# Kernel tuning notes

Measured on AMD Instinct MI355X. Metric: run time of the kernel, lower is better.

The kernel has to match this reference:

```python
import jax, jax.numpy as jnp
import numpy as np

N = 50000


def cheb_conv(x, row, col, deg_inv_sqrt, diag_w, W, b):
    """PyG ChebConv with K=3, normalization='sym', lambda_max=2.
    L~ = 2L/lambda_max - I = -D^{-1/2} A D^{-1/2} (diag 0 for deg>0, -1 for isolated).
    T0 = x, T1 = L~ x, T2 = 2 L~ T1 - T0; out = sum_k Tk @ W[k] + b.
    """
    w = -deg_inv_sqrt[row] * deg_inv_sqrt[col]  # [E]

    def Lhat(h):
        # message: w_e * h[src], aggregated at dst (source_to_target flow)
        agg = jax.ops.segment_sum(w[:, None] * h[col], row, num_segments=N)
        return agg + diag_w[:, None] * h

    Tx0 = x
    Tx1 = Lhat(x)
    Tx2 = 2.0 * Lhat(Tx1) - Tx0
    return Tx0 @ W[0] + Tx1 @ W[1] + Tx2 @ W[2] + b


def setup_inputs() -> dict:
    key = jax.random.key(0)
    ks = jax.random.split(key, 8)
    x = jax.random.normal(ks[0], (N, 512), dtype=jnp.float32)
    edge_index = jax.random.randint(ks[1], (2, 1600000), 0, N, dtype=jnp.int64)
    w1 = jax.random.normal(ks[2], (3, 512, 250), dtype=jnp.float32) * 0.05
    b1 = jnp.zeros((250,), dtype=jnp.float32)
    w2 = jax.random.normal(ks[3], (3, 250, 500), dtype=jnp.float32) * 0.05
    b2 = jnp.zeros((500,), dtype=jnp.float32)
    w3 = jax.random.normal(ks[4], (3, 500, 1000), dtype=jnp.float32) * 0.05
    b3 = jnp.zeros((1000,), dtype=jnp.float32)
    return {"x": x, "edge_index": edge_index, "w1": w1, "b1": b1,
            "w2": w2, "b2": b2, "w3": w3, "b3": b3}


def reference(x, edge_index, w1, b1, w2, b2, w3, b3):
    row, col = edge_index[1], edge_index[0]  # dst, src (source_to_target)
    # symmetric-normalization degree (computed as in PyG get_laplacian: scatter on row)
    deg = jax.ops.segment_sum(jnp.ones(edge_index.shape[1], dtype=x.dtype), row,
                              num_segments=N)
    deg_inv_sqrt = jnp.where(deg > 0, jax.lax.rsqrt(jnp.maximum(deg, 1.0)), 0.0)
    diag_w = jnp.where(deg > 0, 0.0, -1.0).astype(x.dtype)  # 2*L_ii/lmax - 1

    h = jax.nn.relu(cheb_conv(x, row, col, deg_inv_sqrt, diag_w, w1, b1))
    h = jax.nn.relu(cheb_conv(h, row, col, deg_inv_sqrt, diag_w, w2, b2))
    h = jax.nn.relu(cheb_conv(h, row, col, deg_inv_sqrt, diag_w, w3, b3))
    return h
```

## Files before the change

### kernel.cpp

```cpp
#include <hip/hip_runtime.h>


typedef unsigned short u16;
typedef __attribute__((ext_vector_type(8))) short s16x8;
typedef __attribute__((ext_vector_type(4))) float f32x4;
typedef __attribute__((ext_vector_type(8))) unsigned short u16x8;
typedef __attribute__((ext_vector_type(4))) unsigned short u16x4;
typedef __attribute__((ext_vector_type(8))) signed char s8x8;
typedef __attribute__((ext_vector_type(4))) signed char s8x4;

__device__ __forceinline__ float b2f(u16 u) {
  union { unsigned int i; float f; } x; x.i = ((unsigned int)u) << 16; return x.f;
}
__device__ __forceinline__ u16 f2b(float f) {
  union { float f; unsigned int i; } x; x.f = f;
  unsigned int r = x.i + 0x7fffu + ((x.i >> 16) & 1u);
  return (u16)(r >> 16);
}

typedef __attribute__((address_space(1))) unsigned int gu32_t;
typedef __attribute__((address_space(3))) unsigned int lu32_t;
__device__ __forceinline__ void gload16(const void* g, void* l) {
  __builtin_amdgcn_global_load_lds((const gu32_t*)g, (lu32_t*)l, 16, 0, 0);
}

__global__ void k_zero_i32(int* p, int n) {
  int t = blockIdx.x * 256 + threadIdx.x;
  if (t < n) p[t] = 0;
}

__global__ void k_hist(const int* __restrict__ ei, int* __restrict__ cnt, int E) {
  int e = blockIdx.x * 256 + threadIdx.x;
  if (e < E) atomicAdd(&cnt[ei[E + e]], 1);
}

__global__ void k_dis(const int* __restrict__ cnt, float* __restrict__ dis, int N) {
  int t = blockIdx.x * 256 + threadIdx.x;
  if (t < N) dis[t] = cnt[t] > 0 ? rsqrtf((float)cnt[t]) : 0.f;
}

__global__ void k_scan1(const int* __restrict__ cnt, int* __restrict__ part, int N) {
  __shared__ int s[256];
  int t = threadIdx.x, idx = blockIdx.x * 256 + t;
  s[t] = idx < N ? cnt[idx] : 0;
  __syncthreads();
  for (int o = 128; o > 0; o >>= 1) {
    if (t < o) s[t] += s[t + o];
    __syncthreads();
  }
  if (t == 0) part[blockIdx.x] = s[0];
}

__global__ void k_scan2(int* part, int nb, int* csroff, int N, int E) {
  if (threadIdx.x == 0 && blockIdx.x == 0) {
    int run = 0;
    for (int b = 0; b < nb; ++b) { int v = part[b]; part[b] = run; run += v; }
    csroff[N] = E;
  }
}

__global__ void k_scan3(const int* __restrict__ cnt, const int* __restrict__ part,
                        int* __restrict__ csroff, int* __restrict__ cursor, int N) {
  __shared__ int s[256];
  int t = threadIdx.x, idx = blockIdx.x * 256 + t;
  int v = idx < N ? cnt[idx] : 0;
  s[t] = v;
  __syncthreads();
  for (int o = 1; o < 256; o <<= 1) {
    int add = t >= o ? s[t - o] : 0;
    __syncthreads();
    s[t] += add;
    __syncthreads();
  }
  if (idx < N) {
    int ex = part[blockIdx.x] + s[t] - v;
    csroff[idx] = ex;
    cursor[idx] = ex;
  }
}

__global__ void k_scatter(const int* __restrict__ ei, int* __restrict__ cursor,
                          int* __restrict__ csrsrc, int E) {
  int e = blockIdx.x * 256 + threadIdx.x;
  if (e >= E) return;
  int s = ei[e];
  int d = ei[E + e];
  int pos = atomicAdd(&cursor[d], 1);
  csrsrc[pos] = s;
}

__global__ void k_convx(const float* __restrict__ x, u16* __restrict__ C, int N, int NPAD) {
  int t = blockIdx.x * 256 + threadIdx.x;
  int row = t >> 6;
  if (row >= NPAD) return;
  int c0 = (t & 63) * 8;
  u16x8 o;
  if (row < N) {
    const float4* p = (const float4*)(x + (size_t)row * 512 + c0);
    float4 a = p[0], b = p[1];
    o[0] = f2b(a.x); o[1] = f2b(a.y); o[2] = f2b(a.z); o[3] = f2b(a.w);
    o[4] = f2b(b.x); o[5] = f2b(b.y); o[6] = f2b(b.z); o[7] = f2b(b.w);
  } else {
#pragma unroll
    for (int j = 0; j < 8; ++j) o[j] = 0;
  }
  *(u16x8*)(C + (size_t)row * 512 + c0) = o;
}

__global__ void k_convw_kblk(const float* __restrict__ W, u16* __restrict__ Wb,
                             int Fin, int Kpad, int Nout) {
  int n = blockIdx.x;
  int ldw = 3 * Kpad;
  for (int kk = threadIdx.x; kk < ldw; kk += 256) {
    int ck = kk / Kpad, k = kk - ck * Kpad;
    float v = (k < Fin && n < Nout) ? W[((size_t)ck * Fin + k) * Nout + n] : 0.f;
    Wb[(size_t)n * ldw + kk] = f2b(v);
  }
}

__global__ void k_convw_nblk(const float* __restrict__ W, u16* __restrict__ Wb,
                             int Nout ) {
  int n = blockIdx.x;
  int ck = n >> 8, j = n & 255;
  for (int k = threadIdx.x; k < 512; k += 256) {
    float v = (j < Nout) ? W[((size_t)ck * 512 + k) * Nout + j] : 0.f;
    Wb[(size_t)n * 512 + k] = f2b(v);
  }
}

template <int FV>
__global__ __launch_bounds__(256) void k_quant(
    const u16* __restrict__ T, int ldt, signed char* __restrict__ Q, int ldq,
    const float* __restrict__ dis, float* __restrict__ qs, float* __restrict__ sc,
    int N) {
  using uvec = typename
      __hip_internal::conditional<FV == 8, u16x8, u16x4>::type;
  using qvec = typename
      __hip_internal::conditional<FV == 8, s8x8, s8x4>::type;
  const int r = blockIdx.x * 4 + (threadIdx.x >> 6);
  if (r >= N) return;
  const int l = threadIdx.x & 63, c0 = l * FV;
  const uvec v = *(const uvec*)(T + (size_t)r * ldt + c0);
  float f[FV];
  float m = 0.f;
#pragma unroll
  for (int j = 0; j < FV; ++j) { f[j] = b2f(v[j]); m = fmaxf(m, fabsf(f[j])); }
#pragma unroll
  for (int o = 32; o > 0; o >>= 1) m = fmaxf(m, __shfl_xor(m, o, 64));
  const float inv = m > 0.f ? 127.f / m : 0.f;
  qvec q;
#pragma unroll
  for (int j = 0; j < FV; ++j) q[j] = (signed char)(int)rintf(f[j] * inv);
  *(qvec*)(Q + (size_t)r * ldq + c0) = q;
  if (l == 0) {
    const float s = m > 0.f ? m * (1.f / 127.f) : 0.f;
    sc[r] = s;
    qs[r] = dis[r] * s;
  }
}

template <int FV, int MODE>
__global__ __launch_bounds__(256) void spmm_q(
    const signed char* __restrict__ Q, int ldq,
    const float* __restrict__ qs, const float* __restrict__ sc,
    const u16* __restrict__ E0, const u16* __restrict__ E1, int lde,
    const float* __restrict__ bias, int nreal,
    u16* __restrict__ O, int ldo,
    const int* __restrict__ off, const int* __restrict__ srcs,
    const float* __restrict__ dis, int N) {
  using uvec = typename
      __hip_internal::conditional<FV == 8, u16x8, u16x4>::type;
  using qvec = typename
      __hip_internal::conditional<FV == 8, s8x8, s8x4>::type;
  const int r = blockIdx.x * 4 + (threadIdx.x >> 6);
  if (r >= N) return;
  const int c0 = (threadIdx.x & 63) * FV;
  const signed char* __restrict__ Qc = Q + c0;
  float acc[FV];
#pragma unroll
  for (int j = 0; j < FV; ++j) acc[j] = 0.f;
  int e = off[r];
  const int e1 = off[r + 1];
  for (; e + 4 <= e1; e += 4) {
    const int s0 = srcs[e], s1 = srcs[e + 1], s2 = srcs[e + 2], s3 = srcs[e + 3];
    const float w0 = qs[s0], w1 = qs[s1], w2 = qs[s2], w3 = qs[s3];
    const qvec v0 = *(const qvec*)(Qc + (size_t)s0 * ldq);
    const qvec v1 = *(const qvec*)(Qc + (size_t)s1 * ldq);
    const qvec v2 = *(const qvec*)(Qc + (size_t)s2 * ldq);
    const qvec v3 = *(const qvec*)(Qc + (size_t)s3 * ldq);
#pragma unroll
    for (int j = 0; j < FV; ++j)
      acc[j] += w0 * (float)v0[j] + w1 * (float)v1[j] +
                w2 * (float)v2[j] + w3 * (float)v3[j];
  }
  for (; e < e1; ++e) {
    const int s0 = srcs[e];
    const float w0 = qs[s0];
    const qvec v0 = *(const qvec*)(Qc + (size_t)s0 * ldq);
#pragma unroll
    for (int j = 0; j < FV; ++j) acc[j] += w0 * (float)v0[j];
  }
  const float disr = dis[r];
  float lap[FV];
#pragma unroll
  for (int j = 0; j < FV; ++j) lap[j] = -disr * acc[j];
  if (disr == 0.f) {
    const float s = sc[r];
    const qvec v = *(const qvec*)(Qc + (size_t)r * ldq);
#pragma unroll
    for (int j = 0; j < FV; ++j) lap[j] -= s * (float)v[j];
  }
  uvec o;
  if constexpr (MODE == 0) {
#pragma unroll
    for (int j = 0; j < FV; ++j) o[j] = f2b(lap[j]);
  } else if constexpr (MODE == 1) {
    const uvec h = *(const uvec*)(E0 + (size_t)r * lde + c0);
#pragma unroll
    for (int j = 0; j < FV; ++j) o[j] = f2b(2.f * lap[j] - b2f(h[j]));
  } else if constexpr (MODE == 2) {
    const uvec u1 = *(const uvec*)(E0 + (size_t)r * lde + c0);
#pragma unroll
    for (int j = 0; j < FV; ++j) o[j] = f2b(b2f(u1[j]) + 2.f * lap[j]);
  } else {
    const uvec u0 = *(const uvec*)(E0 + (size_t)r * lde + c0);
    const uvec u2 = *(const uvec*)(E1 + (size_t)r * lde + c0);
#pragma unroll
    for (int j = 0; j < FV; ++j) {
      const int c = c0 + j;
      const float bv = (c < nreal) ? bias[c] : 0.f;
      float v = b2f(u0[j]) - b2f(u2[j]) + lap[j] + bv;
      o[j] = f2b(v > 0.f ? v : 0.f);
    }
  }
  *(uvec*)(O + (size_t)r * ldo + c0) = o;
}

template <typename OUTT, bool ACT>
__global__ __launch_bounds__(256) void gemm_k(
    const u16* __restrict__ A, int lda,
    const u16* __restrict__ B, int ldb,
    const float* __restrict__ bias,
    OUTT* __restrict__ C, int ldc,
    int K, int nmask, int nreal, int Nrows, int NT) {
  __shared__ u16 As[128 * 64];
  __shared__ u16 Bs[128 * 64];
  const int tid = threadIdx.x;
  const int w = tid >> 6, l = tid & 63;

  const int nwg = gridDim.x;
  const int q = nwg >> 3, r8 = nwg & 7;
  const int xcd = blockIdx.x & 7, idx = blockIdx.x >> 3;
  const int wg = (xcd < r8 ? xcd * (q + 1) : r8 * (q + 1) + (xcd - r8) * q) + idx;
  const int m0 = (wg / NT) * 128, n0 = (wg % NT) * 128;

  const int srow = w * 8 + (l >> 3);
  const int scol = ((l & 7) ^ (l >> 3)) * 8;
  const u16* ga = A + (size_t)m0 * lda + scol;
  const u16* gb = B + (size_t)n0 * ldb + scol;
  u16* lAs = &As[w * 512];
  u16* lBs = &Bs[w * 512];

  f32x4 acc[4][4];
#pragma unroll
  for (int m = 0; m < 4; ++m)
#pragma unroll
    for (int n = 0; n < 4; ++n) acc[m][n] = (f32x4){0.f, 0.f, 0.f, 0.f};

  const int wr = (w >> 1) * 64, wc = (w & 1) * 64;
  const int tr = l & 15, tg = l >> 4;
  const int rx = tr & 7;

  for (int k0 = 0; k0 < K; k0 += 64) {
    __syncthreads();
#pragma unroll
    for (int c = 0; c < 4; ++c) {
      gload16(ga + (size_t)(srow + c * 32) * lda + k0, lAs + c * 2048);
      gload16(gb + (size_t)(srow + c * 32) * ldb + k0, lBs + c * 2048);
    }
    __syncthreads();
#pragma unroll
    for (int kk = 0; kk < 64; kk += 32) {
      s16x8 af[4], bf[4];
#pragma unroll
      for (int m = 0; m < 4; ++m)
        af[m] = *(const s16x8*)&As[(wr + m * 16 + tr) * 64 + ((((kk >> 3) + tg) ^ rx) * 8)];
#pragma unroll
      for (int n = 0; n < 4; ++n)
        bf[n] = *(const s16x8*)&Bs[(wc + n * 16 + tr) * 64 + ((((kk >> 3) + tg) ^ rx) * 8)];
#pragma unroll
      for (int m = 0; m < 4; ++m)
#pragma unroll
        for (int n = 0; n < 4; ++n)
          acc[m][n] = __builtin_amdgcn_mfma_f32_16x16x32_bf16(af[m], bf[n], acc[m][n], 0, 0, 0);
    }
  }

#pragma unroll
  for (int m = 0; m < 4; ++m) {
    const int gr0 = m0 + wr + m * 16 + tg * 4;
#pragma unroll
    for (int n = 0; n < 4; ++n) {
      const int gc = n0 + wc + n * 16 + tr;
      const bool cv = (gc & nmask) < nreal;
      const float bv = (ACT && cv) ? bias[gc] : 0.f;
#pragma unroll
      for (int j = 0; j < 4; ++j) {
        float v = acc[m][n][j] + bv;
        if (ACT) v = v > 0.f ? v : 0.f;
        if constexpr (sizeof(OUTT) == 2) {
          C[(size_t)(gr0 + j) * ldc + gc] = cv ? f2b(v) : (u16)0;
        } else {
          if (gr0 + j < Nrows && cv)
            C[(size_t)(gr0 + j) * ldc + gc] = v;
        }
      }
    }
  }
}

extern "C" void kernel_launch(void* const* d_in, const int* in_sizes, int n_in,
                              void* d_out, int out_size, void* d_ws, size_t ws_size,
                              hipStream_t stream) {
  const float* x = (const float*)d_in[0];
  const int* ei = (const int*)d_in[1];
  const float* w1 = (const float*)d_in[2];
  const float* b1 = (const float*)d_in[3];
  const float* w2 = (const float*)d_in[4];
  const float* b2 = (const float*)d_in[5];
  const float* w3 = (const float*)d_in[6];
  const float* b3 = (const float*)d_in[7];
  float* out = (float*)d_out;

  const int N = in_sizes[0] / 512;
  const int E = in_sizes[1] / 2;
  const int NPAD = ((N + 127) / 128) * 128;
  const int NB = (N + 255) / 256;
  const int EB = (E + 255) / 256;
  const int MT = NPAD / 128;

  char* ws = (char*)d_ws;
  size_t o = 0;
  auto alloc = [&](size_t b) -> void* {
    void* p = ws + o;
    o = (o + b + 255) & ~(size_t)255;
    return p;
  };
  int* cnt = (int*)alloc((size_t)N * 4);
  float* dis = (float*)alloc((size_t)N * 4);
  int* csroff = (int*)alloc((size_t)(N + 1) * 4);
  int* cursor = (int*)alloc((size_t)N * 4);
  int* part = (int*)alloc(1024);
  float* qs = (float*)alloc((size_t)N * 4);
  float* sc = (float*)alloc((size_t)N * 4);
  int* csrsrc = (int*)alloc((size_t)E * 4);
  u16* CB = (u16*)alloc((size_t)NPAD * 768 * 2);
  u16* CA = (u16*)alloc((size_t)NPAD * 1536 * 2);
  u16* XB = CA;
  u16* U  = CA + (size_t)NPAD * 512;
  u16* P  = U  + (size_t)NPAD * 768;
  u16* Wb = (u16*)alloc((size_t)1024 * 1536 * 2);
  signed char* Q8 = (signed char*)d_out;
  (void)ws_size; (void)n_in; (void)out_size;

  k_zero_i32<<<NB, 256, 0, stream>>>(cnt, N);
  k_hist<<<EB, 256, 0, stream>>>(ei, cnt, E);
  k_dis<<<NB, 256, 0, stream>>>(cnt, dis, N);
  k_scan1<<<NB, 256, 0, stream>>>(cnt, part, N);
  k_scan2<<<1, 64, 0, stream>>>(part, NB, csroff, N, E);
  k_scan3<<<NB, 256, 0, stream>>>(cnt, part, csroff, cursor, N);
  k_scatter<<<EB, 256, 0, stream>>>(ei, cursor, csrsrc, E);

  const int SG = (N + 3) / 4;

  k_convx<<<NPAD / 4, 256, 0, stream>>>(x, XB, N, NPAD);
  k_convw_nblk<<<768, 256, 0, stream>>>(w1, Wb, 250);
  gemm_k<u16, false><<<MT * 6, 256, 0, stream>>>(XB, 512, Wb, 512, nullptr,
                                                 U, 768, 512, 255, 250, N, 6);
  k_quant<4><<<SG, 256, 0, stream>>>(U + 512, 768, Q8, 256, dis, qs, sc, N);
  spmm_q<4, 2><<<SG, 256, 0, stream>>>(Q8, 256, qs, sc, U + 256, (const u16*)nullptr, 768,
                                       nullptr, 0, P, 256, csroff, csrsrc, dis, N);
  k_quant<4><<<SG, 256, 0, stream>>>(P, 256, Q8, 256, dis, qs, sc, N);
  spmm_q<4, 3><<<SG, 256, 0, stream>>>(Q8, 256, qs, sc, U, U + 512, 768,
                                       b1, 250, CB, 768, csroff, csrsrc, dis, N);

  k_convw_kblk<<<512, 256, 0, stream>>>(w2, Wb, 250, 256, 500);
  k_quant<4><<<SG, 256, 0, stream>>>(CB, 768, Q8, 256, dis, qs, sc, N);
  spmm_q<4, 0><<<SG, 256, 0, stream>>>(Q8, 256, qs, sc, (const u16*)nullptr, (const u16*)nullptr, 0,
                                       nullptr, 0, CB + 256, 768, csroff, csrsrc, dis, N);
  k_quant<4><<<SG, 256, 0, stream>>>(CB + 256, 768, Q8, 256, dis, qs, sc, N);
  spmm_q<4, 1><<<SG, 256, 0, stream>>>(Q8, 256, qs, sc, CB, (const u16*)nullptr, 768,
                                       nullptr, 0, CB + 512, 768, csroff, csrsrc, dis, N);
  gemm_k<u16, true><<<MT * 4, 256, 0, stream>>>(CB, 768, Wb, 768, b2,
                                                CA, 1536, 768, 511, 500, N, 4);

  k_convw_kblk<<<1024, 256, 0, stream>>>(w3, Wb, 500, 512, 1000);
  k_quant<8><<<SG, 256, 0, stream>>>(CA, 1536, Q8, 512, dis, qs, sc, N);
  spmm_q<8, 0><<<SG, 256, 0, stream>>>(Q8, 512, qs, sc, (const u16*)nullptr, (const u16*)nullptr, 0,
                                       nullptr, 0, CA + 512, 1536, csroff, csrsrc, dis, N);
  k_quant<8><<<SG, 256, 0, stream>>>(CA + 512, 1536, Q8, 512, dis, qs, sc, N);
  spmm_q<8, 1><<<SG, 256, 0, stream>>>(Q8, 512, qs, sc, CA, (const u16*)nullptr, 1536,
                                       nullptr, 0, CA + 1024, 1536, csroff, csrsrc, dis, N);
  gemm_k<float, true><<<MT * 8, 256, 0, stream>>>(CA, 1536, Wb, 1536, b3,
                                                  out, 1000, 1536, 1023, 1000, N, 8);
}
```

Before: 1.443 ms.

## Replace 128x128 GEMM with double-buffered 256x256 8-wave pipelined kernel

Swaps the single-buffered 128x128 tile GEMM (4 waves, two barriers per k-step) for a 256x256 tile kernel with 8 waves. It double-buffers LDS and interleaves global-to-LDS prefetch of the next k-tiles with MFMA sub-blocks, using explicit vmcnt waits and s_setprio. The aim is more data reuse per tile and latency hidden behind MFMA work. In exchange it uses more LDS and registers, and the larger tiles add padding waste and give fewer workgroups for the narrow layer-1 GEMM.

```diff
diff --git a/kernel.cpp b/kernel.cpp
--- a/kernel.cpp
+++ b/kernel.cpp
@@ -237,76 +237,128 @@
 }
 
 template <typename OUTT, bool ACT>
-__global__ __launch_bounds__(256) void gemm_k(
+__global__ __launch_bounds__(512, 2) void gemm8(
     const u16* __restrict__ A, int lda,
     const u16* __restrict__ B, int ldb,
     const float* __restrict__ bias,
     OUTT* __restrict__ C, int ldc,
     int K, int nmask, int nreal, int Nrows, int NT) {
-  __shared__ u16 As[128 * 64];
-  __shared__ u16 Bs[128 * 64];
+  __shared__ u16 sh[2][2][2][8192];
   const int tid = threadIdx.x;
-  const int w = tid >> 6, l = tid & 63;
+  const int wv = tid >> 6, ln = tid & 63;
 
   const int nwg = gridDim.x;
-  const int q = nwg >> 3, r8 = nwg & 7;
-  const int xcd = blockIdx.x & 7, idx = blockIdx.x >> 3;
-  const int wg = (xcd < r8 ? xcd * (q + 1) : r8 * (q + 1) + (xcd - r8) * q) + idx;
-  const int m0 = (wg / NT) * 128, n0 = (wg % NT) * 128;
-
-  const int srow = w * 8 + (l >> 3);
-  const int scol = ((l & 7) ^ (l >> 3)) * 8;
-  const u16* ga = A + (size_t)m0 * lda + scol;
-  const u16* gb = B + (size_t)n0 * ldb + scol;
-  u16* lAs = &As[w * 512];
-  u16* lBs = &Bs[w * 512];
-
-  f32x4 acc[4][4];
-#pragma unroll
-  for (int m = 0; m < 4; ++m)
-#pragma unroll
-    for (int n = 0; n < 4; ++n) acc[m][n] = (f32x4){0.f, 0.f, 0.f, 0.f};
-
-  const int wr = (w >> 1) * 64, wc = (w & 1) * 64;
-  const int tr = l & 15, tg = l >> 4;
-  const int rx = tr & 7;
-
-  for (int k0 = 0; k0 < K; k0 += 64) {
-    __syncthreads();
-#pragma unroll
-    for (int c = 0; c < 4; ++c) {
-      gload16(ga + (size_t)(srow + c * 32) * lda + k0, lAs + c * 2048);
-      gload16(gb + (size_t)(srow + c * 32) * ldb + k0, lBs + c * 2048);
-    }
-    __syncthreads();
-#pragma unroll
-    for (int kk = 0; kk < 64; kk += 32) {
-      s16x8 af[4], bf[4];
-#pragma unroll
-      for (int m = 0; m < 4; ++m)
-        af[m] = *(const s16x8*)&As[(wr + m * 16 + tr) * 64 + ((((kk >> 3) + tg) ^ rx) * 8)];
-#pragma unroll
-      for (int n = 0; n < 4; ++n)
-        bf[n] = *(const s16x8*)&Bs[(wc + n * 16 + tr) * 64 + ((((kk >> 3) + tg) ^ rx) * 8)];
-#pragma unroll
-      for (int m = 0; m < 4; ++m)
-#pragma unroll
-        for (int n = 0; n < 4; ++n)
-          acc[m][n] = __builtin_amdgcn_mfma_f32_16x16x32_bf16(af[m], bf[n], acc[m][n], 0, 0, 0);
-    }
-  }
-
-#pragma unroll
-  for (int m = 0; m < 4; ++m) {
-    const int gr0 = m0 + wr + m * 16 + tg * 4;
-#pragma unroll
-    for (int n = 0; n < 4; ++n) {
-      const int gc = n0 + wc + n * 16 + tr;
+  const int qq = nwg >> 3, r8 = nwg & 7;
+  const int xcd = blockIdx.x & 7, bidx = blockIdx.x >> 3;
+  const int wg = (xcd < r8 ? xcd * (qq + 1) : r8 * (qq + 1) + (xcd - r8) * qq) + bidx;
+  const int m0 = (wg / NT) * 256, n0 = (wg % NT) * 256;
+
+  const int wm = wv >> 2, wn = wv & 3;
+  const int tr = ln & 15, tg = ln >> 4, rx = tr & 7;
+
+  const int srow = tid >> 3;
+  const int sgr = (tid & 7) ^ (srow & 7);
+  const u16* gA = A + (size_t)(m0 + srow) * lda + sgr * 8;
+  const u16* gB = B + (size_t)(n0 + srow) * ldb + sgr * 8;
+
+  f32x4 acc[8][4];
+#pragma unroll
+  for (int mf = 0; mf < 8; ++mf)
+#pragma unroll
+    for (int nf = 0; nf < 4; ++nf) acc[mf][nf] = (f32x4){0.f, 0.f, 0.f, 0.f};
+  s16x8 fa[8], fb0[4], fb1[4];
+
+  auto SA = [&](int b, int kt, int h) {
+    const u16* s = gA + (size_t)h * 128 * lda + kt * 64;
+    u16* d = &sh[b][0][h][wv * 512];
+    gload16(s, d);
+    gload16(s + (size_t)64 * lda, d + 4096);
+  };
+  auto SB = [&](int b, int kt, int h) {
+    const u16* s = gB + (size_t)h * 128 * ldb + kt * 64;
+    u16* d = &sh[b][1][h][wv * 512];
+    gload16(s, d);
+    gload16(s + (size_t)64 * ldb, d + 4096);
+  };
+  auto LDA_ = [&](int b, int mh) {
+    const u16* base = &sh[b][0][wm][0];
+#pragma unroll
+    for (int mf = 0; mf < 4; ++mf)
+#pragma unroll
+      for (int kx = 0; kx < 2; ++kx) {
+        const int row = mh * 64 + mf * 16 + tr;
+        fa[mf * 2 + kx] = *(const s16x8*)&base[row * 64 + (((kx * 4 + tg) ^ rx) * 8)];
+      }
+  };
+  auto LDB_ = [&](int b, int nh, s16x8* fb) {
+    const u16* base = &sh[b][1][wn >> 1][0];
+#pragma unroll
+    for (int nf = 0; nf < 2; ++nf)
+#pragma unroll
+      for (int kx = 0; kx < 2; ++kx) {
+        const int row = (wn & 1) * 64 + (nh * 2 + nf) * 16 + tr;
+        fb[nf * 2 + kx] = *(const s16x8*)&base[row * 64 + (((kx * 4 + tg) ^ rx) * 8)];
+      }
+  };
+  auto MM = [&](int mh, int nh, const s16x8* fb) {
+    __builtin_amdgcn_s_setprio(1);
+#pragma unroll
+    for (int kx = 0; kx < 2; ++kx)
+#pragma unroll
+      for (int mf = 0; mf < 4; ++mf)
+#pragma unroll
+        for (int nf = 0; nf < 2; ++nf)
+          acc[mh * 4 + mf][nh * 2 + nf] = __builtin_amdgcn_mfma_f32_16x16x32_bf16(
+              fa[mf * 2 + kx], fb[nf * 2 + kx], acc[mh * 4 + mf][nh * 2 + nf], 0, 0, 0);
+    __builtin_amdgcn_s_setprio(0);
+  };
+#define BAR8() { __builtin_amdgcn_s_barrier(); asm volatile("" ::: "memory"); }
+#define VC4() asm volatile("s_waitcnt vmcnt(4)" ::: "memory")
+
+  const int nkt = K >> 6;
+  SA(0, 0, 0); SA(0, 0, 1); SB(0, 0, 0); SB(0, 0, 1);
+  SA(1, 1, 0); SA(1, 1, 1);
+  VC4();
+  BAR8();
+  for (int i = 0; i < (nkt >> 1); ++i) {
+    const int t1 = 2 * i + 1, t2 = 2 * i + 2, t3 = 2 * i + 3;
+    LDA_(0, 0); LDB_(0, 0, fb0);
+    SB(1, t1, 0); SB(1, t1, 1);
+    BAR8(); MM(0, 0, fb0); BAR8();
+    LDB_(0, 1, fb1);
+    BAR8(); MM(0, 1, fb1); BAR8();
+    LDA_(0, 1);
+    BAR8(); MM(1, 1, fb1); BAR8();
+    if (t2 < nkt) { SA(0, t2, 0); SA(0, t2, 1); }
+    BAR8(); MM(1, 0, fb0);
+    VC4();
+    BAR8();
+    LDA_(1, 0); LDB_(1, 0, fb0);
+    if (t2 < nkt) { SB(0, t2, 0); SB(0, t2, 1); }
+    BAR8(); MM(0, 0, fb0); BAR8();
+    LDB_(1, 1, fb1);
+    BAR8(); MM(0, 1, fb1); BAR8();
+    LDA_(1, 1);
+    BAR8(); MM(1, 1, fb1); BAR8();
+    if (t3 < nkt) { SA(1, t3, 0); SA(1, t3, 1); }
+    BAR8(); MM(1, 0, fb0);
+    VC4();
+    BAR8();
+  }
+#undef BAR8
+#undef VC4
+
+#pragma unroll
+  for (int mf = 0; mf < 8; ++mf) {
+    const int gr0 = m0 + wm * 128 + mf * 16 + tg * 4;
+#pragma unroll
+    for (int nf = 0; nf < 4; ++nf) {
+      const int gc = n0 + wn * 64 + nf * 16 + tr;
       const bool cv = (gc & nmask) < nreal;
       const float bv = (ACT && cv) ? bias[gc] : 0.f;
 #pragma unroll
       for (int j = 0; j < 4; ++j) {
-        float v = acc[m][n][j] + bv;
+        float v = acc[mf][nf][j] + bv;
         if (ACT) v = v > 0.f ? v : 0.f;
         if constexpr (sizeof(OUTT) == 2) {
           C[(size_t)(gr0 + j) * ldc + gc] = cv ? f2b(v) : (u16)0;
@@ -334,10 +386,10 @@
 
   const int N = in_sizes[0] / 512;
   const int E = in_sizes[1] / 2;
-  const int NPAD = ((N + 127) / 128) * 128;
+  const int NPAD2 = ((N + 255) / 256) * 256;
   const int NB = (N + 255) / 256;
   const int EB = (E + 255) / 256;
-  const int MT = NPAD / 128;
+  const int MT2 = NPAD2 / 256;
 
   char* ws = (char*)d_ws;
   size_t o = 0;
@@ -354,11 +406,11 @@
   float* qs = (float*)alloc((size_t)N * 4);
   float* sc = (float*)alloc((size_t)N * 4);
   int* csrsrc = (int*)alloc((size_t)E * 4);
-  u16* CB = (u16*)alloc((size_t)NPAD * 768 * 2);
-  u16* CA = (u16*)alloc((size_t)NPAD * 1536 * 2);
+  u16* CB = (u16*)alloc((size_t)NPAD2 * 768 * 2);
+  u16* CA = (u16*)alloc((size_t)NPAD2 * 1536 * 2);
   u16* XB = CA;
-  u16* U  = CA + (size_t)NPAD * 512;
-  u16* P  = U  + (size_t)NPAD * 768;
+  u16* U  = CA + (size_t)NPAD2 * 512;
+  u16* P  = U  + (size_t)NPAD2 * 768;
   u16* Wb = (u16*)alloc((size_t)1024 * 1536 * 2);
   signed char* Q8 = (signed char*)d_out;
   (void)ws_size; (void)n_in; (void)out_size;
@@ -373,10 +425,10 @@
 
   const int SG = (N + 3) / 4;
 
-  k_convx<<<NPAD / 4, 256, 0, stream>>>(x, XB, N, NPAD);
+  k_convx<<<NPAD2 / 4, 256, 0, stream>>>(x, XB, N, NPAD2);
   k_convw_nblk<<<768, 256, 0, stream>>>(w1, Wb, 250);
-  gemm_k<u16, false><<<MT * 6, 256, 0, stream>>>(XB, 512, Wb, 512, nullptr,
-                                                 U, 768, 512, 255, 250, N, 6);
+  gemm8<u16, false><<<MT2 * 3, 512, 0, stream>>>(XB, 512, Wb, 512, nullptr,
+                                                 U, 768, 512, 255, 250, N, 3);
   k_quant<4><<<SG, 256, 0, stream>>>(U + 512, 768, Q8, 256, dis, qs, sc, N);
   spmm_q<4, 2><<<SG, 256, 0, stream>>>(Q8, 256, qs, sc, U + 256, (const u16*)nullptr, 768,
                                        nullptr, 0, P, 256, csroff, csrsrc, dis, N);
@@ -391,8 +443,8 @@
   k_quant<4><<<SG, 256, 0, stream>>>(CB + 256, 768, Q8, 256, dis, qs, sc, N);
   spmm_q<4, 1><<<SG, 256, 0, stream>>>(Q8, 256, qs, sc, CB, (const u16*)nullptr, 768,
                                        nullptr, 0, CB + 512, 768, csroff, csrsrc, dis, N);
-  gemm_k<u16, true><<<MT * 4, 256, 0, stream>>>(CB, 768, Wb, 768, b2,
-                                                CA, 1536, 768, 511, 500, N, 4);
+  gemm8<u16, true><<<MT2 * 2, 512, 0, stream>>>(CB, 768, Wb, 768, b2,
+                                                CA, 1536, 768, 511, 500, N, 2);
 
   k_convw_kblk<<<1024, 256, 0, stream>>>(w3, Wb, 500, 512, 1000);
   k_quant<8><<<SG, 256, 0, stream>>>(CA, 1536, Q8, 512, dis, qs, sc, N);
@@ -401,6 +453,6 @@
   k_quant<8><<<SG, 256, 0, stream>>>(CA + 512, 1536, Q8, 512, dis, qs, sc, N);
   spmm_q<8, 1><<<SG, 256, 0, stream>>>(Q8, 512, qs, sc, CA, (const u16*)nullptr, 1536,
                                        nullptr, 0, CA + 1024, 1536, csroff, csrsrc, dis, N);
-  gemm_k<float, true><<<MT * 8, 256, 0, stream>>>(CA, 1536, Wb, 1536, b3,
-                                                  out, 1000, 1536, 1023, 1000, N, 8);
-}
+  gemm8<float, true><<<MT2 * 4, 512, 0, stream>>>(CA, 1536, Wb, 1536, b3,
+                                                  out, 1000, 1536, 1023, 1000, N, 4);
+}
```

Measured after the change: 1.434 ms. About the same (-0.7%).
